# Performance work log

Hardware: AMD Instinct MI355X
Metric: run time of the kernel (lower is better)

Reference implementation:

```python
import jax, jax.numpy as jnp
import numpy as np

GROUPS = 32
EPS = 1e-5
NUM_HEADS = 8


def group_norm(x, gamma, beta):
    B, C, H, W = x.shape
    xg = x.reshape(B, GROUPS, C // GROUPS, H, W)
    mean = xg.mean(axis=(2, 3, 4), keepdims=True)
    var = xg.var(axis=(2, 3, 4), keepdims=True)
    xg = (xg - mean) * jax.lax.rsqrt(var + EPS)
    x = xg.reshape(B, C, H, W)
    return x * gamma[None, :, None, None] + beta[None, :, None, None]


def setup_inputs() -> dict:
    key = jax.random.key(0)
    k1, k2, k3 = jax.random.split(key, 3)
    C = 512
    x = jax.random.normal(k1, (16, C, 32, 32), dtype=jnp.float32)
    gn_gamma = jnp.ones((C,), dtype=jnp.float32)
    gn_beta = jnp.zeros((C,), dtype=jnp.float32)
    w_qkv = jax.random.normal(k2, (3 * C, C), dtype=jnp.float32) * 0.02
    b_qkv = jnp.zeros((3 * C,), dtype=jnp.float32)
    w_proj = jax.random.normal(k3, (C, C), dtype=jnp.float32) * 0.02
    b_proj = jnp.zeros((C,), dtype=jnp.float32)
    return {"x": x, "gn_gamma": gn_gamma, "gn_beta": gn_beta,
            "w_qkv": w_qkv, "b_qkv": b_qkv, "w_proj": w_proj, "b_proj": b_proj}


def reference(x, gn_gamma, gn_beta, w_qkv, b_qkv, w_proj, b_proj):
    B, C, H, W = x.shape
    nh = NUM_HEADS
    hd = C // nh
    h = group_norm(x, gn_gamma, gn_beta)
    # 1x1 conv == channel matmul: [B,3C,H,W]
    qkv = jnp.einsum('bchw,oc->bohw', h, w_qkv) + b_qkv[None, :, None, None]
    qkv = qkv.reshape(B, 3, nh, hd, H * W)
    q, k, v = qkv[:, 0], qkv[:, 1], qkv[:, 2]  # [B, nh, hd, HW]
    scale = hd ** -0.5
    # attn[b,n,i,j] = sum_d q[b,n,d,i] * k[b,n,d,j]
    attn = jax.nn.softmax(jnp.einsum('bndi,bndj->bnij', q, k) * scale, axis=-1)
    # h[b,n,d,i] = sum_j v[b,n,d,j] * attn[b,n,i,j]
    h = jnp.einsum('bndj,bnij->bndi', v, attn).reshape(B, C, H, W)
    out = jnp.einsum('bchw,oc->bohw', h, w_proj) + b_proj[None, :, None, None]
    return x + out
```

## Files before the change

kernel.cpp:

```cpp
#include <hip/hip_runtime.h>

typedef __bf16 bf16;
typedef __bf16 bf16x2 __attribute__((ext_vector_type(2)));
typedef __bf16 bf16x4 __attribute__((ext_vector_type(4)));
typedef __bf16 bf16x8 __attribute__((ext_vector_type(8)));
typedef float  f32x4  __attribute__((ext_vector_type(4)));
typedef float  f32x16 __attribute__((ext_vector_type(16)));
typedef unsigned int u32x4 __attribute__((ext_vector_type(4)));

#define MFMA32(a,b,c) __builtin_amdgcn_mfma_f32_32x32x16_bf16((a),(b),(c),0,0,0)

#if __has_builtin(__builtin_amdgcn_exp2f)
#define EXP2(x) __builtin_amdgcn_exp2f(x)
#else
#define EXP2(x) exp2f(x)
#endif

__device__ __forceinline__ void gll16(const void* g, void* l) {
  __builtin_amdgcn_global_load_lds((const __attribute__((address_space(1))) unsigned int*)g,
                                   (__attribute__((address_space(3))) unsigned int*)l, 16, 0, 0);
}

__device__ __forceinline__ unsigned pk2(float a, float b) {
  bf16x2 t = { (bf16)a, (bf16)b };
  return __builtin_bit_cast(unsigned, t);
}

__device__ __forceinline__ void pl32swap(unsigned &x, unsigned &y) {
  asm("v_permlane32_swap_b32 %0, %1" : "+v"(x), "+v"(y));
}

static constexpr int Cc = 512;
static constexpr int Ss = 1024;
#define QSCALE 0.18033688011112042f

__global__ __launch_bounds__(256) void k_wconv(const float* __restrict__ wq, const float* __restrict__ wp,
                                               bf16* __restrict__ wqb, bf16* __restrict__ wpb) {
  const int i = blockIdx.x * 256 + threadIdx.x;
  if (i * 4 < 786432) {
    float4 v = ((const float4*)wq)[i];
    bf16x4 o = { (bf16)v.x, (bf16)v.y, (bf16)v.z, (bf16)v.w };
    ((bf16x4*)wqb)[i] = o;
  } else {
    const int j = i - 786432 / 4;
    float4 v = ((const float4*)wp)[j];
    bf16x4 o = { (bf16)v.x, (bf16)v.y, (bf16)v.z, (bf16)v.w };
    ((bf16x4*)wpb)[j] = o;
  }
}

__global__ __launch_bounds__(256, 2) void k_gnorm(const float* __restrict__ x,
                                                  const float* __restrict__ gamma,
                                                  const float* __restrict__ beta,
                                                  bf16* __restrict__ ht) {
  const int g = blockIdx.x;
  const int b = blockIdx.y;
  const float* base = x + ((size_t)b * Cc + g * 16) * Ss;
  const int tid = threadIdx.x;

  f32x4 xr[16];
  float s = 0.f, sq = 0.f;
  #pragma unroll
  for (int k = 0; k < 16; ++k) {
    xr[k] = ((const f32x4*)base)[k * 256 + tid];
    s  += xr[k][0] + xr[k][1] + xr[k][2] + xr[k][3];
    sq += xr[k][0] * xr[k][0] + xr[k][1] * xr[k][1] + xr[k][2] * xr[k][2] + xr[k][3] * xr[k][3];
  }
  #pragma unroll
  for (int m = 1; m < 64; m <<= 1) { s += __shfl_xor(s, m); sq += __shfl_xor(sq, m); }
  __shared__ float red[8];
  if ((tid & 63) == 0) { red[tid >> 6] = s; red[4 + (tid >> 6)] = sq; }
  __syncthreads();
  const float stot = red[0] + red[1] + red[2] + red[3];
  const float sqt  = red[4] + red[5] + red[6] + red[7];
  const float mean = stot * (1.f / 16384.f);
  const float var  = sqt * (1.f / 16384.f) - mean * mean;
  const float rstd = rsqrtf(var + 1e-5f);

  float ga[16], bb[16];
  #pragma unroll
  for (int k = 0; k < 16; ++k) {
    ga[k] = gamma[g * 16 + k] * rstd;
    bb[k] = beta[g * 16 + k] - mean * ga[k];
  }

  bf16* dst0 = ht + ((size_t)b * Ss + tid * 4) * Cc + g * 16;
  #pragma unroll
  for (int j = 0; j < 4; ++j) {
    bf16x8 o0, o1;
    #pragma unroll
    for (int k = 0; k < 8; ++k)  o0[k] = (bf16)(xr[k][j] * ga[k] + bb[k]);
    #pragma unroll
    for (int k = 0; k < 8; ++k)  o1[k] = (bf16)(xr[8 + k][j] * ga[8 + k] + bb[8 + k]);
    bf16* d = dst0 + (size_t)j * Cc;
    *(bf16x8*)d = o0;
    *(bf16x8*)(d + 8) = o1;
  }
}

template<int MODE>
__global__ __launch_bounds__(256, 2) void k_gemm(const bf16* __restrict__ Aw,
                                                 const bf16* __restrict__ Bt,
                                                 const float* __restrict__ bias,
                                                 bf16* __restrict__ qo, bf16* __restrict__ ko,
                                                 bf16* __restrict__ vo,
                                                 const float* __restrict__ xres,
                                                 float* __restrict__ out) {
  const int nt = blockIdx.x, mt = blockIdx.y, b = blockIdx.z;
  const int M0 = mt * 128, N0 = nt * 128;
  __shared__ __align__(16) bf16 lA[2][16 * 512];
  __shared__ __align__(16) bf16 lB[2][16 * 512];
  const int tid = threadIdx.x;
  const int l = tid & 63, w = tid >> 6;
  const int wm = w >> 1, wn = w & 1;
  const int l31 = l & 31, h = l >> 5;
  const int ct = tid >> 6;
  const bf16* Bb = Bt + (size_t)b * Ss * Cc;

  const char* asrc = (const char*)(Aw + (size_t)(M0 + l31) * 512 + ct * 16 + h * 8);
  const char* bsrc = (const char*)(Bb + (size_t)(N0 + l31) * 512 + ct * 16 + h * 8);
  const int dstoff = ct * 1024 + l * 16;

  f32x16 acc[2][2];
  #pragma unroll
  for (int i = 0; i < 2; ++i)
    #pragma unroll
    for (int j = 0; j < 2; ++j)
      #pragma unroll
      for (int r = 0; r < 16; ++r) acc[i][j][r] = 0.f;

  #pragma unroll
  for (int mb = 0; mb < 4; ++mb)
    gll16(asrc + (size_t)mb * 32768, (char*)lA[0] + dstoff + mb * 4096);
  #pragma unroll
  for (int nb = 0; nb < 4; ++nb)
    gll16(bsrc + (size_t)nb * 32768, (char*)lB[0] + dstoff + nb * 4096);

  #pragma unroll
  for (int kt = 0; kt < 8; ++kt) {
    const int cur = kt & 1;
    if (kt < 7) {
      #pragma unroll
      for (int mb = 0; mb < 4; ++mb)
        gll16(asrc + (size_t)mb * 32768 + (kt + 1) * 128, (char*)lA[cur ^ 1] + dstoff + mb * 4096);
      #pragma unroll
      for (int nb = 0; nb < 4; ++nb)
        gll16(bsrc + (size_t)nb * 32768 + (kt + 1) * 128, (char*)lB[cur ^ 1] + dstoff + nb * 4096);
      asm volatile("s_waitcnt vmcnt(8)" ::: "memory");
    } else {
      asm volatile("s_waitcnt vmcnt(0)" ::: "memory");
    }
    __builtin_amdgcn_s_barrier();
    __builtin_amdgcn_sched_barrier(0);

    __builtin_amdgcn_s_setprio(1);
    #pragma unroll
    for (int kb = 0; kb < 4; ++kb) {
      bf16x8 a0 = *(const bf16x8*)((const char*)lA[cur] + ((wm * 2 + 0) * 4 + kb) * 1024 + l * 16);
      bf16x8 a1 = *(const bf16x8*)((const char*)lA[cur] + ((wm * 2 + 1) * 4 + kb) * 1024 + l * 16);
      bf16x8 b0 = *(const bf16x8*)((const char*)lB[cur] + ((wn * 2 + 0) * 4 + kb) * 1024 + l * 16);
      bf16x8 b1 = *(const bf16x8*)((const char*)lB[cur] + ((wn * 2 + 1) * 4 + kb) * 1024 + l * 16);
      acc[0][0] = MFMA32(a0, b0, acc[0][0]);
      acc[0][1] = MFMA32(a0, b1, acc[0][1]);
      acc[1][0] = MFMA32(a1, b0, acc[1][0]);
      acc[1][1] = MFMA32(a1, b1, acc[1][1]);
    }
    __builtin_amdgcn_s_setprio(0);
    if (kt < 7) {
      asm volatile("s_waitcnt lgkmcnt(0)" ::: "memory");
      __builtin_amdgcn_s_barrier();
    }
  }

  #pragma unroll
  for (int m = 0; m < 2; ++m) {
    const int ofr = M0 + wm * 64 + m * 32;
    #pragma unroll
    for (int n = 0; n < 2; ++n) {
      const int sI = N0 + wn * 64 + n * 32 + l31;
      #pragma unroll
      for (int Qi = 0; Qi < 4; ++Qi) {
        const int rb = Qi * 8 + h * 4;
        float v[4], bi[4];
        #pragma unroll
        for (int r = 0; r < 4; ++r) {
          v[r] = acc[m][n][Qi * 4 + r];
          bi[r] = bias[ofr + rb + r];
        }
        if (MODE == 0) {
          const int which = ofr >> 9;
          const int nh = (ofr >> 6) & 7;
          const int dbase = (ofr & 63) + rb;
          const size_t bh = (size_t)b * 8 + nh;
          if (which == 2) {
            #pragma unroll
            for (int r = 0; r < 4; ++r)
              vo[(bh * 64 + dbase + r) * 1024 + sI] = (bf16)(v[r] + bi[r]);
          } else {
            const float qs = which ? 1.f : QSCALE;
            bf16x4 pk = { (bf16)((v[0] + bi[0]) * qs), (bf16)((v[1] + bi[1]) * qs),
                          (bf16)((v[2] + bi[2]) * qs), (bf16)((v[3] + bi[3]) * qs) };
            bf16* dst = (which ? ko : qo) + (bh * 1024 + sI) * 64 + dbase;
            *(bf16x4*)dst = pk;
          }
        } else {
          #pragma unroll
          for (int r = 0; r < 4; ++r) {
            const size_t idx = ((size_t)b * 512 + ofr + rb + r) * 1024 + sI;
            out[idx] = xres[idx] + bi[r] + v[r];
          }
        }
      }
    }
  }
}

__global__ __launch_bounds__(512, 3) void k_attn(const bf16* __restrict__ qT,
                                                 const bf16* __restrict__ kT,
                                                 const bf16* __restrict__ vv,
                                                 bf16* __restrict__ ao) {
  const int it = blockIdx.x, nh = blockIdx.y, b = blockIdx.z;
  const size_t bh = (size_t)b * 8 + nh;
  const char* kh = (const char*)(kT + bh * 65536);
  const char* vh = (const char*)(vv + bh * 65536);
  __shared__ __align__(16) char smem[32768];
  const int tid = threadIdx.x;
  const int w = tid >> 6, l = tid & 63;
  const int l31 = l & 31, h = l >> 5;

  const int ct = tid >> 6, c3 = ct & 3, c2 = ct >> 2;
  const char* ksrc = kh + (size_t)(c2 * 32 + l31) * 128 + c3 * 32 + h * 16;
  const char* vsrc = vh + (size_t)(c2 * 32 + l31) * 2048 + c3 * 32 + h * 16;
  char* lkdst = smem + tid * 16;
  char* lvdst = smem + 16384 + tid * 16;

  const bf16* qrow = qT + bh * 65536 + (size_t)(it * 256 + w * 32 + l31) * 64;
  bf16x8 qf[4];
  #pragma unroll
  for (int kq = 0; kq < 4; ++kq) qf[kq] = *(const bf16x8*)(qrow + kq * 16 + h * 8);

  gll16(ksrc, lkdst);
  gll16(vsrc, lvdst);

  f32x16 oacc[2];
  #pragma unroll
  for (int dt = 0; dt < 2; ++dt)
    #pragma unroll
    for (int r = 0; r < 16; ++r) oacc[dt][r] = 0.f;
  float lacc0 = 0.f, lacc1 = 0.f;

  __syncthreads();

  int cur = 0;
  for (int t = 0; t < 16; ++t) {
    if (t < 15) {
      gll16(ksrc + (size_t)(t + 1) * 8192, lkdst + (cur ^ 1) * 8192);
      gll16(vsrc + (size_t)(t + 1) * 128,  lvdst + (cur ^ 1) * 8192);
    }
    const char* lkc = smem + cur * 8192;
    const char* lvc = smem + 16384 + cur * 8192;

    f32x16 sf[2];
    #pragma unroll
    for (int r = 0; r < 16; ++r) { sf[0][r] = 0.f; sf[1][r] = 0.f; }
    __builtin_amdgcn_s_setprio(1);
    #pragma unroll
    for (int kq = 0; kq < 4; ++kq) {
      bf16x8 a0 = *(const bf16x8*)(lkc + kq * 1024 + l * 16);
      bf16x8 a1 = *(const bf16x8*)(lkc + (4 + kq) * 1024 + l * 16);
      sf[0] = MFMA32(a0, qf[kq], sf[0]);
      sf[1] = MFMA32(a1, qf[kq], sf[1]);
    }
    __builtin_amdgcn_s_setprio(0);

    unsigned pw[2][4][2];
    #pragma unroll
    for (int jt = 0; jt < 2; ++jt) {
      #pragma unroll
      for (int Qi = 0; Qi < 4; ++Qi) {
        const float p0 = EXP2(sf[jt][Qi * 4 + 0]);
        const float p1 = EXP2(sf[jt][Qi * 4 + 1]);
        const float p2 = EXP2(sf[jt][Qi * 4 + 2]);
        const float p3 = EXP2(sf[jt][Qi * 4 + 3]);
        lacc0 += p0 + p1; lacc1 += p2 + p3;
        pw[jt][Qi][0] = pk2(p0, p1);
        pw[jt][Qi][1] = pk2(p2, p3);
      }
    }

    bf16x8 pb[4];
    #pragma unroll
    for (int s = 0; s < 4; ++s) {
      const int jt = s >> 1, sq = s & 1;
      unsigned x0 = pw[jt][2 * sq][0], y0 = pw[jt][2 * sq + 1][0];
      unsigned x1 = pw[jt][2 * sq][1], y1 = pw[jt][2 * sq + 1][1];
      pl32swap(x0, y0);
      pl32swap(x1, y1);
      u32x4 wv = { x0, x1, y0, y1 };
      pb[s] = __builtin_bit_cast(bf16x8, wv);
    }

    __builtin_amdgcn_s_setprio(1);
    #pragma unroll
    for (int dt = 0; dt < 2; ++dt) {
      #pragma unroll
      for (int s = 0; s < 4; ++s) {
        bf16x8 av = *(const bf16x8*)(lvc + (dt * 4 + s) * 1024 + l * 16);
        oacc[dt] = MFMA32(av, pb[s], oacc[dt]);
      }
    }
    __builtin_amdgcn_s_setprio(0);
    __syncthreads();
    cur ^= 1;
  }

  float ls = lacc0 + lacc1;
  ls += __shfl_xor(ls, 32);
  const float rinv = 1.f / ls;

  bf16* aor = ao + ((size_t)b * 1024 + it * 256 + w * 32 + l31) * 512 + nh * 64;
  #pragma unroll
  for (int dt = 0; dt < 2; ++dt) {
    #pragma unroll
    for (int Qi = 0; Qi < 4; ++Qi) {
      bf16x4 o = { (bf16)(oacc[dt][Qi * 4 + 0] * rinv), (bf16)(oacc[dt][Qi * 4 + 1] * rinv),
                   (bf16)(oacc[dt][Qi * 4 + 2] * rinv), (bf16)(oacc[dt][Qi * 4 + 3] * rinv) };
      *(bf16x4*)(aor + dt * 32 + Qi * 8 + h * 4) = o;
    }
  }
}

extern "C" void kernel_launch(void* const* d_in, const int* in_sizes, int n_in,
                              void* d_out, int out_size, void* d_ws, size_t ws_size,
                              hipStream_t stream) {
  (void)in_sizes; (void)n_in; (void)out_size; (void)ws_size;
  const float* x   = (const float*)d_in[0];
  const float* gam = (const float*)d_in[1];
  const float* bet = (const float*)d_in[2];
  const float* wq  = (const float*)d_in[3];
  const float* bq  = (const float*)d_in[4];
  const float* wp  = (const float*)d_in[5];
  const float* bp  = (const float*)d_in[6];
  float* out = (float*)d_out;

  bf16* ws  = (bf16*)d_ws;
  bf16* ht  = ws;
  bf16* qT  = ws + 8388608;
  bf16* kT  = ws + 16777216;
  bf16* vv  = ws + 25165824;
  bf16* wqb = ws + 33554432;
  bf16* wpb = ws + 34340864;

  k_wconv<<<1024, 256, 0, stream>>>(wq, wp, wqb, wpb);
  k_gnorm<<<dim3(32, 16), 256, 0, stream>>>(x, gam, bet, ht);
  k_gemm<0><<<dim3(8, 12, 16), 256, 0, stream>>>(wqb, ht, bq, qT, kT, vv, nullptr, nullptr);
  k_attn<<<dim3(4, 8, 16), 512, 0, stream>>>(qT, kT, vv, ht);
  k_gemm<1><<<dim3(8, 4, 16), 256, 0, stream>>>(wpb, ht, bp, nullptr, nullptr, nullptr, x, out);
}
```

Measured before the change: 150.2 us.

## Enlarge GEMM tile to 256x128 with swizzled LDS layout and K=32 steps

The GEMM kernel now computes 256x128 output tiles per block, so each wave holds 4x2 MFMA accumulators instead of 2x2. Loads move K in chunks of 32 over 16 iterations, using an XOR-swizzled row-major LDS layout. The aim is more operand reuse per LDS byte and fewer redundant B-tile loads, with grids halved in the M dimension to match. In exchange there are more registers per thread, fewer blocks in flight, and twice as many barrier iterations.

```diff
diff --git a/kernel.cpp b/kernel.cpp
--- a/kernel.cpp
+++ b/kernel.cpp
@@ -107,46 +107,48 @@
                                                  const float* __restrict__ xres,
                                                  float* __restrict__ out) {
   const int nt = blockIdx.x, mt = blockIdx.y, b = blockIdx.z;
-  const int M0 = mt * 128, N0 = nt * 128;
-  __shared__ __align__(16) bf16 lA[2][16 * 512];
-  __shared__ __align__(16) bf16 lB[2][16 * 512];
+  const int M0 = mt * 256, N0 = nt * 128;
+  __shared__ __align__(16) char lds[2][24576];
   const int tid = threadIdx.x;
   const int l = tid & 63, w = tid >> 6;
   const int wm = w >> 1, wn = w & 1;
   const int l31 = l & 31, h = l >> 5;
-  const int ct = tid >> 6;
   const bf16* Bb = Bt + (size_t)b * Ss * Cc;
 
-  const char* asrc = (const char*)(Aw + (size_t)(M0 + l31) * 512 + ct * 16 + h * 8);
-  const char* bsrc = (const char*)(Bb + (size_t)(N0 + l31) * 512 + ct * 16 + h * 8);
-  const int dstoff = ct * 1024 + l * 16;
-
-  f32x16 acc[2][2];
-  #pragma unroll
-  for (int i = 0; i < 2; ++i)
+  const int r4 = tid >> 2;
+  const int csw = ((tid & 3) ^ (r4 & 3)) * 16;
+  const char* asrc = (const char*)Aw + (size_t)(M0 + r4) * 1024 + csw;
+  const char* bsrc = (const char*)Bb + (size_t)(N0 + r4) * 1024 + csw;
+  const int dstoff = tid * 16;
+
+  f32x16 acc[4][2];
+  #pragma unroll
+  for (int i = 0; i < 4; ++i)
     #pragma unroll
     for (int j = 0; j < 2; ++j)
       #pragma unroll
       for (int r = 0; r < 16; ++r) acc[i][j][r] = 0.f;
 
-  #pragma unroll
-  for (int mb = 0; mb < 4; ++mb)
-    gll16(asrc + (size_t)mb * 32768, (char*)lA[0] + dstoff + mb * 4096);
-  #pragma unroll
-  for (int nb = 0; nb < 4; ++nb)
-    gll16(bsrc + (size_t)nb * 32768, (char*)lB[0] + dstoff + nb * 4096);
-
-  #pragma unroll
-  for (int kt = 0; kt < 8; ++kt) {
+  const int sw3 = l31 & 3;
+
+  #pragma unroll
+  for (int p = 0; p < 4; ++p)
+    gll16(asrc + (size_t)p * 65536, (char*)lds[0] + dstoff + p * 4096);
+  #pragma unroll
+  for (int p = 0; p < 2; ++p)
+    gll16(bsrc + (size_t)p * 65536, (char*)lds[0] + 16384 + dstoff + p * 4096);
+
+  #pragma unroll
+  for (int kt = 0; kt < 16; ++kt) {
     const int cur = kt & 1;
-    if (kt < 7) {
-      #pragma unroll
-      for (int mb = 0; mb < 4; ++mb)
-        gll16(asrc + (size_t)mb * 32768 + (kt + 1) * 128, (char*)lA[cur ^ 1] + dstoff + mb * 4096);
-      #pragma unroll
-      for (int nb = 0; nb < 4; ++nb)
-        gll16(bsrc + (size_t)nb * 32768 + (kt + 1) * 128, (char*)lB[cur ^ 1] + dstoff + nb * 4096);
-      asm volatile("s_waitcnt vmcnt(8)" ::: "memory");
+    if (kt < 15) {
+      #pragma unroll
+      for (int p = 0; p < 4; ++p)
+        gll16(asrc + (size_t)p * 65536 + (kt + 1) * 64, (char*)lds[cur ^ 1] + dstoff + p * 4096);
+      #pragma unroll
+      for (int p = 0; p < 2; ++p)
+        gll16(bsrc + (size_t)p * 65536 + (kt + 1) * 64, (char*)lds[cur ^ 1] + 16384 + dstoff + p * 4096);
+      asm volatile("s_waitcnt vmcnt(6)" ::: "memory");
     } else {
       asm volatile("s_waitcnt vmcnt(0)" ::: "memory");
     }
@@ -155,36 +157,45 @@
 
     __builtin_amdgcn_s_setprio(1);
     #pragma unroll
-    for (int kb = 0; kb < 4; ++kb) {
-      bf16x8 a0 = *(const bf16x8*)((const char*)lA[cur] + ((wm * 2 + 0) * 4 + kb) * 1024 + l * 16);
-      bf16x8 a1 = *(const bf16x8*)((const char*)lA[cur] + ((wm * 2 + 1) * 4 + kb) * 1024 + l * 16);
-      bf16x8 b0 = *(const bf16x8*)((const char*)lB[cur] + ((wn * 2 + 0) * 4 + kb) * 1024 + l * 16);
-      bf16x8 b1 = *(const bf16x8*)((const char*)lB[cur] + ((wn * 2 + 1) * 4 + kb) * 1024 + l * 16);
-      acc[0][0] = MFMA32(a0, b0, acc[0][0]);
-      acc[0][1] = MFMA32(a0, b1, acc[0][1]);
-      acc[1][0] = MFMA32(a1, b0, acc[1][0]);
-      acc[1][1] = MFMA32(a1, b1, acc[1][1]);
+    for (int kb = 0; kb < 2; ++kb) {
+      const int cb16 = ((kb * 2 + h) ^ sw3) * 16;
+      bf16x8 af[4], bfr[2];
+      #pragma unroll
+      for (int mb = 0; mb < 4; ++mb) {
+        const int row = wm * 128 + mb * 32 + l31;
+        af[mb] = *(const bf16x8*)((const char*)lds[cur] + row * 64 + cb16);
+      }
+      #pragma unroll
+      for (int nb = 0; nb < 2; ++nb) {
+        const int row = wn * 64 + nb * 32 + l31;
+        bfr[nb] = *(const bf16x8*)((const char*)lds[cur] + 16384 + row * 64 + cb16);
+      }
+      #pragma unroll
+      for (int mb = 0; mb < 4; ++mb)
+        #pragma unroll
+        for (int nb = 0; nb < 2; ++nb)
+          acc[mb][nb] = MFMA32(af[mb], bfr[nb], acc[mb][nb]);
     }
     __builtin_amdgcn_s_setprio(0);
-    if (kt < 7) {
+    if (kt < 15) {
       asm volatile("s_waitcnt lgkmcnt(0)" ::: "memory");
       __builtin_amdgcn_s_barrier();
     }
   }
 
   #pragma unroll
-  for (int m = 0; m < 2; ++m) {
-    const int ofr = M0 + wm * 64 + m * 32;
-    #pragma unroll
-    for (int n = 0; n < 2; ++n) {
-      const int sI = N0 + wn * 64 + n * 32 + l31;
+  for (int mb = 0; mb < 4; ++mb) {
+    const int ofr = M0 + wm * 128 + mb * 32;
+    #pragma unroll
+    for (int nb = 0; nb < 2; ++nb) {
+      const int sI = N0 + wn * 64 + nb * 32 + l31;
       #pragma unroll
       for (int Qi = 0; Qi < 4; ++Qi) {
         const int rb = Qi * 8 + h * 4;
         float v[4], bi[4];
         #pragma unroll
         for (int r = 0; r < 4; ++r) {
-          v[r] = acc[m][n][Qi * 4 + r];
+          v[r] = acc[mb][nb][Qi * 4 + r];
           bi[r] = bias[ofr + rb + r];
         }
         if (MODE == 0) {
@@ -353,7 +364,7 @@
 
   k_wconv<<<1024, 256, 0, stream>>>(wq, wp, wqb, wpb);
   k_gnorm<<<dim3(32, 16), 256, 0, stream>>>(x, gam, bet, ht);
-  k_gemm<0><<<dim3(8, 12, 16), 256, 0, stream>>>(wqb, ht, bq, qT, kT, vv, nullptr, nullptr);
+  k_gemm<0><<<dim3(8, 6, 16), 256, 0, stream>>>(wqb, ht, bq, qT, kT, vv, nullptr, nullptr);
   k_attn<<<dim3(4, 8, 16), 512, 0, stream>>>(qT, kT, vv, ht);
-  k_gemm<1><<<dim3(8, 4, 16), 256, 0, stream>>>(wpb, ht, bp, nullptr, nullptr, nullptr, x, out);
-}
+  k_gemm<1><<<dim3(8, 2, 16), 256, 0, stream>>>(wpb, ht, bp, nullptr, nullptr, nullptr, x, out);
+}
```

Result: faster. 137.6 us (-8.4%).
